# Kernel tuning notes

Measured on AMD Instinct MI355X. Metric: run time of the kernel, lower is better.

## Reference

```python
import jax, jax.numpy as jnp
import numpy as np

B, N, C, H = 2, 2048, 256, 8
HD = C // H  # 32


def _pairwise_sq_dist(x, y):
    # x,y: [B,N,3] -> [B,N,N] squared euclidean distance
    x2 = jnp.sum(x * x, axis=-1)  # [B,N]
    y2 = jnp.sum(y * y, axis=-1)  # [B,N]
    xy = jnp.einsum('bnd,bmd->bnm', x, y)
    return x2[:, :, None] + y2[:, None, :] - 2.0 * xy


def setup_inputs() -> dict:
    key = jax.random.key(0)
    ks = jax.random.split(key, 12)
    s = 0.02
    return {
        'feature': jax.random.normal(ks[0], (B, N, C), jnp.float32),
        'points': jax.random.normal(ks[1], (B, N, 3), jnp.float32),
        'Wq': jax.random.normal(ks[2], (C, H * HD), jnp.float32) * s,
        'bq': jnp.zeros((H * HD,), jnp.float32),
        'Wk': jax.random.normal(ks[3], (C, H * HD), jnp.float32) * s,
        'bk': jnp.zeros((H * HD,), jnp.float32),
        'Wv': jax.random.normal(ks[4], (C, H * HD), jnp.float32) * s,
        'bv': jnp.zeros((H * HD,), jnp.float32),
        'Wo': jax.random.normal(ks[5], (H * HD, C), jnp.float32) * s,
        'bo': jnp.zeros((C,), jnp.float32),
        'ln_g': jnp.ones((C,), jnp.float32),
        'ln_b': jnp.zeros((C,), jnp.float32),
    }


def reference(feature, points, Wq, bq, Wk, bk, Wv, bv, Wo, bo, ln_g, ln_b):
    xyz = points[..., 0:3]
    dist = _pairwise_sq_dist(xyz, xyz)  # [B,N,N] geometric bias

    q = (feature @ Wq + bq).reshape(B, N, H, HD)
    k = (feature @ Wk + bk).reshape(B, N, H, HD)
    v = (feature @ Wv + bv).reshape(B, N, H, HD)

    # distance-biased multi-head attention (Geoglobal_FPT)
    logits = jnp.einsum('bnhd,bmhd->bhnm', q, k) / jnp.sqrt(jnp.float32(HD))
    logits = logits - dist[:, None, :, :]  # closer points attend more
    attn = jax.nn.softmax(logits, axis=-1)
    out = jnp.einsum('bhnm,bmhd->bnhd', attn, v).reshape(B, N, H * HD)
    out = out @ Wo + bo

    # residual + post-LayerNorm
    f = feature + out
    mu = jnp.mean(f, axis=-1, keepdims=True)
    var = jnp.mean(jnp.square(f - mu), axis=-1, keepdims=True)
    f = (f - mu) * jax.lax.rsqrt(var + 1e-5) * ln_g + ln_b
    return f
```

## Files before the change

kernel.cpp:

```cpp
#include <hip/hip_runtime.h>
#include <hip/hip_bf16.h>

#define B_ 2
#define N_ 2048
#define C_ 256
#define H_ 8
#define HD_ 32

typedef __bf16 bhalf;
typedef bhalf bhalf8 __attribute__((ext_vector_type(8)));
typedef bhalf bhalf4 __attribute__((ext_vector_type(4)));
typedef float floatx4 __attribute__((ext_vector_type(4)));
typedef short short4v __attribute__((ext_vector_type(4)));

__device__ __forceinline__ floatx4 mfma16x16x16bf16(bhalf4 a, bhalf4 b, floatx4 c) {
#if __has_builtin(__builtin_amdgcn_mfma_f32_16x16x16_bf16)
    return __builtin_amdgcn_mfma_f32_16x16x16_bf16(a, b, c, 0, 0, 0);
#else
    return __builtin_amdgcn_mfma_f32_16x16x16bf16_1k(
        __builtin_bit_cast(short4v, a), __builtin_bit_cast(short4v, b), c, 0, 0, 0);
#endif
}

__global__ __launch_bounds__(256) void prep_all(
    const float* __restrict__ Wq, const float* __restrict__ Wk,
    const float* __restrict__ Wv, const float* __restrict__ Wo,
    const float* __restrict__ pts, const float* __restrict__ feat,
    bhalf* __restrict__ Wtb, bhalf* __restrict__ qext,
    bhalf* __restrict__ kext, bhalf* __restrict__ fb)
{
    __shared__ float T[64][65];
    const int bx = blockIdx.x;
    const int t = threadIdx.x;
    if (bx < 64) {
        const int wsel = bx >> 4;
        const float* W = wsel == 0 ? Wq : (wsel == 1 ? Wk : (wsel == 2 ? Wv : Wo));
        bhalf* dst = Wtb + (size_t)wsel * (C_ * C_);
        const int tile = bx & 15;
        const int kt = (tile >> 2) * 64, nt = (tile & 3) * 64;
        const int c4 = (t & 15) * 4;
#pragma unroll
        for (int i = 0; i < 4; ++i) {
            const int r = (t >> 4) + i * 16;
            const float4 w = *(const float4*)&W[(kt + r) * C_ + nt + c4];
            T[r][c4 + 0] = w.x; T[r][c4 + 1] = w.y; T[r][c4 + 2] = w.z; T[r][c4 + 3] = w.w;
        }
        __syncthreads();
#pragma unroll
        for (int i = 0; i < 4; ++i) {
            const int n = (t >> 4) + i * 16;
            bhalf4 o;
            o[0] = (bhalf)T[c4 + 0][n]; o[1] = (bhalf)T[c4 + 1][n];
            o[2] = (bhalf)T[c4 + 2][n]; o[3] = (bhalf)T[c4 + 3][n];
            *(bhalf4*)&dst[(nt + n) * C_ + kt + c4] = o;
        }
    } else if (bx < 80) {
        const int i = (bx - 64) * 256 + t;
        const float x = pts[i * 3 + 0], y = pts[i * 3 + 1], z = pts[i * 3 + 2];
        const float nn = x * x + y * y + z * z;
        const bhalf hi = (bhalf)nn;
        const bhalf lo = (bhalf)(nn - (float)hi);
        bhalf8 qe, ke;
        qe[0] = (bhalf)(2.f * x); qe[1] = (bhalf)(2.f * y); qe[2] = (bhalf)(2.f * z);
        qe[3] = (bhalf)(-(float)hi); qe[4] = (bhalf)(-(float)lo);
        qe[5] = (bhalf)1.f; qe[6] = (bhalf)1.f; qe[7] = (bhalf)0.f;
        ke[0] = (bhalf)x; ke[1] = (bhalf)y; ke[2] = (bhalf)z;
        ke[3] = (bhalf)1.f; ke[4] = (bhalf)1.f;
        ke[5] = (bhalf)(-(float)hi); ke[6] = (bhalf)(-(float)lo); ke[7] = (bhalf)0.f;
        *(bhalf8*)&qext[(size_t)i * 8] = qe;
        *(bhalf8*)&kext[(size_t)i * 8] = ke;
    } else {
        const int idx = ((bx - 80) * 256 + t) * 4;
        const float4 f = *(const float4*)&feat[idx];
        bhalf4 o;
        o[0] = (bhalf)f.x; o[1] = (bhalf)f.y; o[2] = (bhalf)f.z; o[3] = (bhalf)f.w;
        *(bhalf4*)&fb[idx] = o;
    }
}

__global__ __launch_bounds__(256) void qkv_gemm(
    const bhalf* __restrict__ fb, const bhalf* __restrict__ Wtb,
    const float* __restrict__ bq, const float* __restrict__ bk,
    const float* __restrict__ bv,
    bhalf* __restrict__ qs, bhalf* __restrict__ kg, bhalf* __restrict__ vt)
{
    __shared__ __align__(16) bhalf Alds[2][32][72];
    __shared__ __align__(16) bhalf Blds[2][64][72];

    const int tid = threadIdx.x;
    const int wave = tid >> 6, lane = tid & 63;
    const int quad = lane >> 4, l16 = lane & 15;
    const int m0 = blockIdx.x * 32;
    const int which = blockIdx.y >> 2;
    const int n0 = (blockIdx.y & 3) * 64;
    const bhalf* Wt = Wtb + (size_t)which * (C_ * C_);
    const int mw = (wave & 1) * 16;
    const int cw = (wave >> 1) * 32;

    const floatx4 zacc = {0.f, 0.f, 0.f, 0.f};
    floatx4 acc[2] = {zacc, zacc};

    const int arow = tid >> 3, aoff = (tid & 7) * 8;
    const int brow = tid >> 2, boff = (tid & 3) * 16;

    bhalf8 ra  = *(const bhalf8*)&fb[(m0 + arow) * C_ + aoff];
    bhalf8 rb0 = *(const bhalf8*)&Wt[(n0 + brow) * C_ + boff];
    bhalf8 rb1 = *(const bhalf8*)&Wt[(n0 + brow) * C_ + boff + 8];
    *(bhalf8*)&Alds[0][arow][aoff] = ra;
    *(bhalf8*)&Blds[0][brow][boff] = rb0;
    *(bhalf8*)&Blds[0][brow][boff + 8] = rb1;

    int cur = 0;
    for (int kci = 0; kci < 4; ++kci) {
        __syncthreads();
        if (kci < 3) {
            const int kc = (kci + 1) * 64;
            ra  = *(const bhalf8*)&fb[(m0 + arow) * C_ + kc + aoff];
            rb0 = *(const bhalf8*)&Wt[(n0 + brow) * C_ + kc + boff];
            rb1 = *(const bhalf8*)&Wt[(n0 + brow) * C_ + kc + boff + 8];
        }
        const bhalf8 a0 = *(const bhalf8*)&Alds[cur][mw + l16][quad * 8];
        const bhalf8 a1 = *(const bhalf8*)&Alds[cur][mw + l16][32 + quad * 8];
#pragma unroll
        for (int f = 0; f < 2; ++f) {
            const bhalf8 b0 = *(const bhalf8*)&Blds[cur][cw + f * 16 + l16][quad * 8];
            const bhalf8 b1 = *(const bhalf8*)&Blds[cur][cw + f * 16 + l16][32 + quad * 8];
            acc[f] = __builtin_amdgcn_mfma_f32_16x16x32_bf16(a0, b0, acc[f], 0, 0, 0);
            acc[f] = __builtin_amdgcn_mfma_f32_16x16x32_bf16(a1, b1, acc[f], 0, 0, 0);
        }
        if (kci < 3) {
            *(bhalf8*)&Alds[cur ^ 1][arow][aoff] = ra;
            *(bhalf8*)&Blds[cur ^ 1][brow][boff] = rb0;
            *(bhalf8*)&Blds[cur ^ 1][brow][boff + 8] = rb1;
        }
        cur ^= 1;
    }

    const float scale = 0.17677669529663687f;
    const float* bias = which == 0 ? bq : (which == 1 ? bk : bv);
#pragma unroll
    for (int f = 0; f < 2; ++f) {
        const int cg = n0 + cw + f * 16 + l16;
        const float bi = bias[cg];
        const int hh = cg >> 5, dd = cg & 31;
#pragma unroll
        for (int r = 0; r < 4; ++r) {
            const int m = m0 + mw + quad * 4 + r;
            const int bb = m >> 11, nn = m & (N_ - 1);
            const float val = acc[f][r] + bi;
            if (which == 0) {
                qs[((size_t)(bb * H_ + hh) * N_ + nn) * HD_ + dd] = (bhalf)(val * scale);
            } else if (which == 1) {
                kg[((size_t)(bb * H_ + hh) * N_ + nn) * HD_ + dd] = (bhalf)val;
            } else {
                vt[(((size_t)(bb * H_ + hh) * (N_ / 64) + (nn >> 6)) * HD_ + dd) * 64 + (nn & 63)] = (bhalf)val;
            }
        }
    }
}

__global__ __launch_bounds__(256) void attn_kernel(
    const bhalf* __restrict__ qs, const bhalf* __restrict__ kg,
    const bhalf* __restrict__ vt, const bhalf* __restrict__ qext,
    const bhalf* __restrict__ kext,
    bhalf* __restrict__ po, float* __restrict__ pl, int spbits)
{
    __shared__ __align__(16) bhalf Ks[2][64][40];
    __shared__ __align__(16) bhalf Vts[2][32][72];
    __shared__ __align__(16) bhalf Kes[2][64][8];

    const int tid = threadIdx.x;
    const int wave = tid >> 6, lane = tid & 63;
    const int quad = lane >> 4, l16 = lane & 15;
    const int n0 = blockIdx.x * 64;
    const int h = blockIdx.y;
    const int sp = blockIdx.z & ((1 << spbits) - 1);
    const int b = blockIdx.z >> spbits;
    const int bh = b * H_ + h;

    const int qrow = n0 + wave * 16 + l16;
    const bhalf8 bq_ = *(const bhalf8*)&qs[((size_t)bh * N_ + qrow) * HD_ + quad * 8];
    bhalf8 zv8;
#pragma unroll
    for (int j = 0; j < 8; ++j) zv8[j] = (bhalf)0.f;
    const bhalf8 bqe = (quad == 0)
        ? *(const bhalf8*)&qext[(size_t)(b * N_ + qrow) * 8] : zv8;

    const floatx4 zacc = {0.f, 0.f, 0.f, 0.f};
    floatx4 o0 = zacc, o1 = zacc;
    float ls = 0.f;

    const int skey = tid >> 2, sseg = tid & 3;
    const int vd = tid >> 3, vks = tid & 7;
    const int ekey = tid >> 1, eoff = (tid & 1) * 4;
    const int iters = (N_ >> spbits) / 64;
    const int mbase = sp * (N_ >> spbits);

    bhalf8 rk = *(const bhalf8*)&kg[((size_t)bh * N_ + mbase + skey) * HD_ + sseg * 8];
    bhalf8 rv = *(const bhalf8*)&vt[(((size_t)bh * (N_ / 64) + (mbase >> 6)) * HD_ + vd) * 64 + vks * 8];
    bhalf4 re;
    if (tid < 128) re = *(const bhalf4*)&kext[(size_t)(b * N_ + mbase + ekey) * 8 + eoff];
    *(bhalf8*)&Ks[0][skey][sseg * 8] = rk;
    *(bhalf8*)&Vts[0][vd][vks * 8] = rv;
    if (tid < 128) *(bhalf4*)&Kes[0][ekey][eoff] = re;

    int cur = 0;
    for (int it = 0; it < iters; ++it) {
        __syncthreads();
        if (it + 1 < iters) {
            const int m1 = mbase + (it + 1) * 64;
            rk = *(const bhalf8*)&kg[((size_t)bh * N_ + m1 + skey) * HD_ + sseg * 8];
            rv = *(const bhalf8*)&vt[(((size_t)bh * (N_ / 64) + (m1 >> 6)) * HD_ + vd) * 64 + vks * 8];
            if (tid < 128) re = *(const bhalf4*)&kext[(size_t)(b * N_ + m1 + ekey) * 8 + eoff];
        }
#pragma unroll
        for (int mt = 0; mt < 4; ++mt) {
            const bhalf8 ak_ = *(const bhalf8*)&Ks[cur][mt * 16 + l16][quad * 8];
            floatx4 st = __builtin_amdgcn_mfma_f32_16x16x32_bf16(ak_, bq_, zacc, 0, 0, 0);
            const bhalf8 ake = (quad == 0)
                ? *(const bhalf8*)&Kes[cur][mt * 16 + l16][0] : zv8;
            st = __builtin_amdgcn_mfma_f32_16x16x32_bf16(ake, bqe, st, 0, 0, 0);
            bhalf4 pt;
#pragma unroll
            for (int r = 0; r < 4; ++r) {
                const float p = __expf(st[r]);
                ls += p;
                pt[r] = (bhalf)p;
            }
            const bhalf4 av0 = *(const bhalf4*)&Vts[cur][l16][mt * 16 + quad * 4];
            const bhalf4 av1 = *(const bhalf4*)&Vts[cur][16 + l16][mt * 16 + quad * 4];
            o0 = mfma16x16x16bf16(av0, pt, o0);
            o1 = mfma16x16x16bf16(av1, pt, o1);
        }
        if (it + 1 < iters) {
            *(bhalf8*)&Ks[cur ^ 1][skey][sseg * 8] = rk;
            *(bhalf8*)&Vts[cur ^ 1][vd][vks * 8] = rv;
            if (tid < 128) *(bhalf4*)&Kes[cur ^ 1][ekey][eoff] = re;
        }
        cur ^= 1;
    }

    ls += __shfl_xor(ls, 16);
    ls += __shfl_xor(ls, 32);

    const size_t pobase = (size_t)sp * ((size_t)B_ * H_ * N_ * HD_) + (size_t)bh * N_ * HD_;
    bhalf4 w0, w1;
#pragma unroll
    for (int r = 0; r < 4; ++r) { w0[r] = (bhalf)o0[r]; w1[r] = (bhalf)o1[r]; }
    *(bhalf4*)&po[pobase + (size_t)qrow * HD_ + quad * 4] = w0;
    *(bhalf4*)&po[pobase + (size_t)qrow * HD_ + 16 + quad * 4] = w1;
    if (lane < 16)
        pl[(size_t)sp * (B_ * H_ * N_) + (size_t)bh * N_ + qrow] = ls;
}

__global__ __launch_bounds__(256) void outln_gemm(
    const bhalf* __restrict__ po, const float* __restrict__ pl,
    const bhalf* __restrict__ Wot, const float* __restrict__ bo,
    const float* __restrict__ feat, const float* __restrict__ g,
    const float* __restrict__ bb, float* __restrict__ out, int splits)
{
    __shared__ __align__(16) bhalf Alds[16][264];
    __shared__ __align__(16) bhalf Blds[2][256][40];
    __shared__ float rden[16][8];
    __shared__ float wsum[4][16][2];
    __shared__ float stats[16][2];

    const int tid = threadIdx.x;
    const int wave = tid >> 6, lane = tid & 63;
    const int quad = lane >> 4, l16 = lane & 15;
    const int row0 = blockIdx.x * 16;

    if (tid < 128) {
        const int m = tid >> 3, hh = tid & 7;
        const int grow = row0 + m;
        const int b = grow >> 11, n = grow & (N_ - 1);
        float den = 0.f;
        for (int sp = 0; sp < splits; ++sp)
            den += pl[(size_t)sp * (B_ * H_ * N_) + (size_t)(b * H_ + hh) * N_ + n];
        rden[m][hh] = 1.f / den;
    }
    __syncthreads();

    {
        const int m = tid >> 4, seg = tid & 15;
        const int hh = seg >> 1, d0 = (seg & 1) * 16;
        const int grow = row0 + m;
        const int b = grow >> 11, n = grow & (N_ - 1);
        const size_t idx = ((size_t)(b * H_ + hh) * N_ + n) * HD_ + d0;
        float num[16];
#pragma unroll
        for (int j = 0; j < 16; ++j) num[j] = 0.f;
        for (int sp = 0; sp < splits; ++sp) {
            const bhalf8 p0 = *(const bhalf8*)&po[(size_t)sp * ((size_t)B_ * H_ * N_ * HD_) + idx];
            const bhalf8 p1 = *(const bhalf8*)&po[(size_t)sp * ((size_t)B_ * H_ * N_ * HD_) + idx + 8];
#pragma unroll
            for (int j = 0; j < 8; ++j) { num[j] += (float)p0[j]; num[8 + j] += (float)p1[j]; }
        }
        const float r = rden[m][hh];
        bhalf8 a0, a1;
#pragma unroll
        for (int j = 0; j < 8; ++j) { a0[j] = (bhalf)(num[j] * r); a1[j] = (bhalf)(num[8 + j] * r); }
        *(bhalf8*)&Alds[m][seg * 16] = a0;
        *(bhalf8*)&Alds[m][seg * 16 + 8] = a1;
    }

    const floatx4 zacc = {0.f, 0.f, 0.f, 0.f};
    floatx4 acc[4];
#pragma unroll
    for (int f = 0; f < 4; ++f) acc[f] = zacc;

    bhalf8 rb0 = *(const bhalf8*)&Wot[tid * C_ + 0];
    bhalf8 rb1 = *(const bhalf8*)&Wot[tid * C_ + 8];
    bhalf8 rb2 = *(const bhalf8*)&Wot[tid * C_ + 16];
    bhalf8 rb3 = *(const bhalf8*)&Wot[tid * C_ + 24];
    *(bhalf8*)&Blds[0][tid][0]  = rb0;
    *(bhalf8*)&Blds[0][tid][8]  = rb1;
    *(bhalf8*)&Blds[0][tid][16] = rb2;
    *(bhalf8*)&Blds[0][tid][24] = rb3;

    int cur = 0;
    for (int kci = 0; kci < 8; ++kci) {
        __syncthreads();
        if (kci < 7) {
            const bhalf* wp = &Wot[tid * C_ + (kci + 1) * 32];
            rb0 = *(const bhalf8*)(wp);
            rb1 = *(const bhalf8*)(wp + 8);
            rb2 = *(const bhalf8*)(wp + 16);
            rb3 = *(const bhalf8*)(wp + 24);
        }
        const bhalf8 af = *(const bhalf8*)&Alds[l16][kci * 32 + quad * 8];
#pragma unroll
        for (int f = 0; f < 4; ++f) {
            const bhalf8 bfr = *(const bhalf8*)&Blds[cur][wave * 64 + f * 16 + l16][quad * 8];
            acc[f] = __builtin_amdgcn_mfma_f32_16x16x32_bf16(af, bfr, acc[f], 0, 0, 0);
        }
        if (kci < 7) {
            *(bhalf8*)&Blds[cur ^ 1][tid][0]  = rb0;
            *(bhalf8*)&Blds[cur ^ 1][tid][8]  = rb1;
            *(bhalf8*)&Blds[cur ^ 1][tid][16] = rb2;
            *(bhalf8*)&Blds[cur ^ 1][tid][24] = rb3;
        }
        cur ^= 1;
    }

    float fv[4][4];
    float s1[4] = {0.f, 0.f, 0.f, 0.f}, s2[4] = {0.f, 0.f, 0.f, 0.f};
#pragma unroll
    for (int f = 0; f < 4; ++f) {
        const int col = wave * 64 + f * 16 + l16;
        const float bic = bo[col];
#pragma unroll
        for (int r = 0; r < 4; ++r) {
            const int m = quad * 4 + r;
            const float x = acc[f][r] + bic + feat[(row0 + m) * C_ + col];
            fv[f][r] = x;
            s1[r] += x; s2[r] += x * x;
        }
    }
#pragma unroll
    for (int r = 0; r < 4; ++r) {
        for (int o = 1; o < 16; o <<= 1) {
            s1[r] += __shfl_xor(s1[r], o);
            s2[r] += __shfl_xor(s2[r], o);
        }
    }
    if (l16 == 0) {
#pragma unroll
        for (int r = 0; r < 4; ++r) {
            wsum[wave][quad * 4 + r][0] = s1[r];
            wsum[wave][quad * 4 + r][1] = s2[r];
        }
    }
    __syncthreads();
    if (tid < 16) {
        float a = 0.f, bsq = 0.f;
#pragma unroll
        for (int w = 0; w < 4; ++w) { a += wsum[w][tid][0]; bsq += wsum[w][tid][1]; }
        const float mu = a * (1.f / C_);
        const float var = bsq * (1.f / C_) - mu * mu;
        stats[tid][0] = mu;
        stats[tid][1] = rsqrtf(var + 1e-5f);
    }
    __syncthreads();
#pragma unroll
    for (int f = 0; f < 4; ++f) {
        const int col = wave * 64 + f * 16 + l16;
        const float gc = g[col], bc = bb[col];
#pragma unroll
        for (int r = 0; r < 4; ++r) {
            const int m = quad * 4 + r;
            out[(row0 + m) * C_ + col] = (fv[f][r] - stats[m][0]) * stats[m][1] * gc + bc;
        }
    }
}

extern "C" void kernel_launch(void* const* d_in, const int* in_sizes, int n_in,
                              void* d_out, int out_size, void* d_ws, size_t ws_size,
                              hipStream_t stream) {
    const float* feat = (const float*)d_in[0];
    const float* pts  = (const float*)d_in[1];
    const float* Wq   = (const float*)d_in[2];
    const float* bq   = (const float*)d_in[3];
    const float* Wk   = (const float*)d_in[4];
    const float* bk   = (const float*)d_in[5];
    const float* Wv   = (const float*)d_in[6];
    const float* bv   = (const float*)d_in[7];
    const float* Wo   = (const float*)d_in[8];
    const float* bo   = (const float*)d_in[9];
    const float* lng  = (const float*)d_in[10];
    const float* lnb  = (const float*)d_in[11];

    char* w = (char*)d_ws;
    bhalf* Wtb  = (bhalf*)(w);
    bhalf* fb   = (bhalf*)(w + 524288);
    bhalf* qs   = (bhalf*)(w + 2621440);
    bhalf* kg   = (bhalf*)(w + 4718592);
    bhalf* vtp  = (bhalf*)(w + 6815744);
    bhalf* qext = (bhalf*)(w + 8912896);
    bhalf* kext = (bhalf*)(w + 8978432);
    float* pl   = (float*)(w + 9043968);
    bhalf* po   = (bhalf*)(w + 9568256);

    const int spbits = (ws_size >= 17956864u) ? 2 : 1;
    const int splits = 1 << spbits;

    prep_all<<<80 + B_ * N_ * C_ / 1024, 256, 0, stream>>>(
        Wq, Wk, Wv, Wo, pts, feat, Wtb, qext, kext, fb);
    qkv_gemm<<<dim3(B_ * N_ / 32, 12), 256, 0, stream>>>(
        fb, Wtb, bq, bk, bv, qs, kg, vtp);
    attn_kernel<<<dim3(N_ / 64, H_, B_ << spbits), 256, 0, stream>>>(
        qs, kg, vtp, qext, kext, po, pl, spbits);
    outln_gemm<<<B_ * N_ / 16, 256, 0, stream>>>(
        po, pl, Wtb + 3 * (C_ * C_), bo, feat, lng, lnb, (float*)d_out, splits);
}
```

Baseline: 125.9 us.

## Process two query tiles per wave in attention and vectorize V stores

Each attention block now covers 128 query rows instead of 64. Each wave computes two 16-row query tiles against the same K/V tiles in shared memory, so every K and V LDS read and global load is reused twice and the grid is halved. Separately, the QKV GEMM epilogue writes the transposed V output as one 4-element vector store instead of four scalar stores. The cost is more accumulator registers per thread and fewer blocks in flight, which could lower occupancy.

```diff
diff --git a/kernel.cpp b/kernel.cpp
--- a/kernel.cpp
+++ b/kernel.cpp
@@ -143,17 +143,21 @@
         const int cg = n0 + cw + f * 16 + l16;
         const float bi = bias[cg];
         const int hh = cg >> 5, dd = cg & 31;
-#pragma unroll
-        for (int r = 0; r < 4; ++r) {
-            const int m = m0 + mw + quad * 4 + r;
-            const int bb = m >> 11, nn = m & (N_ - 1);
-            const float val = acc[f][r] + bi;
-            if (which == 0) {
-                qs[((size_t)(bb * H_ + hh) * N_ + nn) * HD_ + dd] = (bhalf)(val * scale);
-            } else if (which == 1) {
-                kg[((size_t)(bb * H_ + hh) * N_ + nn) * HD_ + dd] = (bhalf)val;
-            } else {
-                vt[(((size_t)(bb * H_ + hh) * (N_ / 64) + (nn >> 6)) * HD_ + dd) * 64 + (nn & 63)] = (bhalf)val;
+        const int m = m0 + mw + quad * 4;
+        const int bb = m >> 11, nn = m & (N_ - 1);
+        if (which == 2) {
+            bhalf4 vw;
+#pragma unroll
+            for (int r = 0; r < 4; ++r) vw[r] = (bhalf)(acc[f][r] + bi);
+            *(bhalf4*)&vt[(((size_t)(bb * H_ + hh) * (N_ / 64) + (nn >> 6)) * HD_ + dd) * 64 + (nn & 63)] = vw;
+        } else {
+#pragma unroll
+            for (int r = 0; r < 4; ++r) {
+                const float val = acc[f][r] + bi;
+                if (which == 0)
+                    qs[((size_t)(bb * H_ + hh) * N_ + nn + r) * HD_ + dd] = (bhalf)(val * scale);
+                else
+                    kg[((size_t)(bb * H_ + hh) * N_ + nn + r) * HD_ + dd] = (bhalf)val;
             }
         }
     }
@@ -172,23 +176,27 @@
     const int tid = threadIdx.x;
     const int wave = tid >> 6, lane = tid & 63;
     const int quad = lane >> 4, l16 = lane & 15;
-    const int n0 = blockIdx.x * 64;
+    const int n0 = blockIdx.x * 128;
     const int h = blockIdx.y;
     const int sp = blockIdx.z & ((1 << spbits) - 1);
     const int b = blockIdx.z >> spbits;
     const int bh = b * H_ + h;
 
-    const int qrow = n0 + wave * 16 + l16;
-    const bhalf8 bq_ = *(const bhalf8*)&qs[((size_t)bh * N_ + qrow) * HD_ + quad * 8];
+    const int qrow0 = n0 + wave * 32 + l16;
+    const int qrow1 = qrow0 + 16;
+    const bhalf8 bq0 = *(const bhalf8*)&qs[((size_t)bh * N_ + qrow0) * HD_ + quad * 8];
+    const bhalf8 bq1 = *(const bhalf8*)&qs[((size_t)bh * N_ + qrow1) * HD_ + quad * 8];
     bhalf8 zv8;
 #pragma unroll
     for (int j = 0; j < 8; ++j) zv8[j] = (bhalf)0.f;
-    const bhalf8 bqe = (quad == 0)
-        ? *(const bhalf8*)&qext[(size_t)(b * N_ + qrow) * 8] : zv8;
+    const bhalf8 bqe0 = (quad == 0)
+        ? *(const bhalf8*)&qext[(size_t)(b * N_ + qrow0) * 8] : zv8;
+    const bhalf8 bqe1 = (quad == 0)
+        ? *(const bhalf8*)&qext[(size_t)(b * N_ + qrow1) * 8] : zv8;
 
     const floatx4 zacc = {0.f, 0.f, 0.f, 0.f};
-    floatx4 o0 = zacc, o1 = zacc;
-    float ls = 0.f;
+    floatx4 o00 = zacc, o01 = zacc, o10 = zacc, o11 = zacc;
+    float ls0 = 0.f, ls1 = 0.f;
 
     const int skey = tid >> 2, sseg = tid & 3;
     const int vd = tid >> 3, vks = tid & 7;
@@ -216,21 +224,26 @@
 #pragma unroll
         for (int mt = 0; mt < 4; ++mt) {
             const bhalf8 ak_ = *(const bhalf8*)&Ks[cur][mt * 16 + l16][quad * 8];
-            floatx4 st = __builtin_amdgcn_mfma_f32_16x16x32_bf16(ak_, bq_, zacc, 0, 0, 0);
             const bhalf8 ake = (quad == 0)
                 ? *(const bhalf8*)&Kes[cur][mt * 16 + l16][0] : zv8;
-            st = __builtin_amdgcn_mfma_f32_16x16x32_bf16(ake, bqe, st, 0, 0, 0);
-            bhalf4 pt;
+            floatx4 st0 = __builtin_amdgcn_mfma_f32_16x16x32_bf16(ak_, bq0, zacc, 0, 0, 0);
+            st0 = __builtin_amdgcn_mfma_f32_16x16x32_bf16(ake, bqe0, st0, 0, 0, 0);
+            floatx4 st1 = __builtin_amdgcn_mfma_f32_16x16x32_bf16(ak_, bq1, zacc, 0, 0, 0);
+            st1 = __builtin_amdgcn_mfma_f32_16x16x32_bf16(ake, bqe1, st1, 0, 0, 0);
+            bhalf4 pt0, pt1;
 #pragma unroll
             for (int r = 0; r < 4; ++r) {
-                const float p = __expf(st[r]);
-                ls += p;
-                pt[r] = (bhalf)p;
+                const float p0 = __expf(st0[r]);
+                const float p1 = __expf(st1[r]);
+                ls0 += p0; ls1 += p1;
+                pt0[r] = (bhalf)p0; pt1[r] = (bhalf)p1;
             }
             const bhalf4 av0 = *(const bhalf4*)&Vts[cur][l16][mt * 16 + quad * 4];
             const bhalf4 av1 = *(const bhalf4*)&Vts[cur][16 + l16][mt * 16 + quad * 4];
-            o0 = mfma16x16x16bf16(av0, pt, o0);
-            o1 = mfma16x16x16bf16(av1, pt, o1);
+            o00 = mfma16x16x16bf16(av0, pt0, o00);
+            o01 = mfma16x16x16bf16(av1, pt0, o01);
+            o10 = mfma16x16x16bf16(av0, pt1, o10);
+            o11 = mfma16x16x16bf16(av1, pt1, o11);
         }
         if (it + 1 < iters) {
             *(bhalf8*)&Ks[cur ^ 1][skey][sseg * 8] = rk;
@@ -240,17 +253,24 @@
         cur ^= 1;
     }
 
-    ls += __shfl_xor(ls, 16);
-    ls += __shfl_xor(ls, 32);
+    ls0 += __shfl_xor(ls0, 16); ls0 += __shfl_xor(ls0, 32);
+    ls1 += __shfl_xor(ls1, 16); ls1 += __shfl_xor(ls1, 32);
 
     const size_t pobase = (size_t)sp * ((size_t)B_ * H_ * N_ * HD_) + (size_t)bh * N_ * HD_;
-    bhalf4 w0, w1;
-#pragma unroll
-    for (int r = 0; r < 4; ++r) { w0[r] = (bhalf)o0[r]; w1[r] = (bhalf)o1[r]; }
-    *(bhalf4*)&po[pobase + (size_t)qrow * HD_ + quad * 4] = w0;
-    *(bhalf4*)&po[pobase + (size_t)qrow * HD_ + 16 + quad * 4] = w1;
+    bhalf4 w00, w01, w10, w11;
+#pragma unroll
+    for (int r = 0; r < 4; ++r) {
+        w00[r] = (bhalf)o00[r]; w01[r] = (bhalf)o01[r];
+        w10[r] = (bhalf)o10[r]; w11[r] = (bhalf)o11[r];
+    }
+    *(bhalf4*)&po[pobase + (size_t)qrow0 * HD_ + quad * 4] = w00;
+    *(bhalf4*)&po[pobase + (size_t)qrow0 * HD_ + 16 + quad * 4] = w01;
+    *(bhalf4*)&po[pobase + (size_t)qrow1 * HD_ + quad * 4] = w10;
+    *(bhalf4*)&po[pobase + (size_t)qrow1 * HD_ + 16 + quad * 4] = w11;
     if (lane < 16)
-        pl[(size_t)sp * (B_ * H_ * N_) + (size_t)bh * N_ + qrow] = ls;
+        pl[(size_t)sp * (B_ * H_ * N_) + (size_t)bh * N_ + qrow0] = ls0;
+    else if (lane < 32)
+        pl[(size_t)sp * (B_ * H_ * N_) + (size_t)bh * N_ + qrow1] = ls1;
 }
 
 __global__ __launch_bounds__(256) void outln_gemm(
@@ -428,7 +448,7 @@
         Wq, Wk, Wv, Wo, pts, feat, Wtb, qext, kext, fb);
     qkv_gemm<<<dim3(B_ * N_ / 32, 12), 256, 0, stream>>>(
         fb, Wtb, bq, bk, bv, qs, kg, vtp);
-    attn_kernel<<<dim3(N_ / 64, H_, B_ << spbits), 256, 0, stream>>>(
+    attn_kernel<<<dim3(N_ / 128, H_, B_ << spbits), 256, 0, stream>>>(
         qs, kg, vtp, qext, kext, po, pl, spbits);
     outln_gemm<<<B_ * N_ / 16, 256, 0, stream>>>(
         po, pl, Wtb + 3 * (C_ * C_), bo, feat, lng, lnb, (float*)d_out, splits);
```

After: 122.1 us. -3.0%, faster.

## Widen attention query tile per block, raise key split count, halve out-LN row tile

Applied to the files above, without the earlier changes.

The attention kernel now has each wave handle 64 query rows (4 groups of 16) instead of 16, so each K/V tile staged in shared memory is reused across 4x more queries. The grid shrinks in x, and the key dimension is split up to 8 ways when workspace allows, to keep parallelism. The output GEMM+LayerNorm kernel uses 8-row blocks with zero padding to spread work over more blocks, and the V store in the QKV GEMM is vectorised to 4-wide. In exchange, register pressure rises from the 8 accumulators per wave, and po/pl traffic plus the reduction grow with more splits.

```diff
diff --git a/kernel.cpp b/kernel.cpp
--- a/kernel.cpp
+++ b/kernel.cpp
@@ -143,17 +143,21 @@
         const int cg = n0 + cw + f * 16 + l16;
         const float bi = bias[cg];
         const int hh = cg >> 5, dd = cg & 31;
-#pragma unroll
-        for (int r = 0; r < 4; ++r) {
-            const int m = m0 + mw + quad * 4 + r;
-            const int bb = m >> 11, nn = m & (N_ - 1);
-            const float val = acc[f][r] + bi;
-            if (which == 0) {
-                qs[((size_t)(bb * H_ + hh) * N_ + nn) * HD_ + dd] = (bhalf)(val * scale);
-            } else if (which == 1) {
-                kg[((size_t)(bb * H_ + hh) * N_ + nn) * HD_ + dd] = (bhalf)val;
-            } else {
-                vt[(((size_t)(bb * H_ + hh) * (N_ / 64) + (nn >> 6)) * HD_ + dd) * 64 + (nn & 63)] = (bhalf)val;
+        const int m = m0 + mw + quad * 4;
+        const int bb = m >> 11, nn = m & (N_ - 1);
+        if (which == 2) {
+            bhalf4 vw;
+#pragma unroll
+            for (int r = 0; r < 4; ++r) vw[r] = (bhalf)(acc[f][r] + bi);
+            *(bhalf4*)&vt[(((size_t)(bb * H_ + hh) * (N_ / 64) + (nn >> 6)) * HD_ + dd) * 64 + (nn & 63)] = vw;
+        } else {
+#pragma unroll
+            for (int r = 0; r < 4; ++r) {
+                const float val = acc[f][r] + bi;
+                if (which == 0)
+                    qs[((size_t)(bb * H_ + hh) * N_ + nn + r) * HD_ + dd] = (bhalf)(val * scale);
+                else
+                    kg[((size_t)(bb * H_ + hh) * N_ + nn + r) * HD_ + dd] = (bhalf)val;
             }
         }
     }
@@ -172,23 +176,30 @@
     const int tid = threadIdx.x;
     const int wave = tid >> 6, lane = tid & 63;
     const int quad = lane >> 4, l16 = lane & 15;
-    const int n0 = blockIdx.x * 64;
+    const int n0 = blockIdx.x * 256;
     const int h = blockIdx.y;
     const int sp = blockIdx.z & ((1 << spbits) - 1);
     const int b = blockIdx.z >> spbits;
     const int bh = b * H_ + h;
 
-    const int qrow = n0 + wave * 16 + l16;
-    const bhalf8 bq_ = *(const bhalf8*)&qs[((size_t)bh * N_ + qrow) * HD_ + quad * 8];
     bhalf8 zv8;
 #pragma unroll
     for (int j = 0; j < 8; ++j) zv8[j] = (bhalf)0.f;
-    const bhalf8 bqe = (quad == 0)
-        ? *(const bhalf8*)&qext[(size_t)(b * N_ + qrow) * 8] : zv8;
+
+    bhalf8 bq[4], bqe[4];
+#pragma unroll
+    for (int g = 0; g < 4; ++g) {
+        const int qrow = n0 + wave * 64 + g * 16 + l16;
+        bq[g] = *(const bhalf8*)&qs[((size_t)bh * N_ + qrow) * HD_ + quad * 8];
+        bqe[g] = (quad == 0)
+            ? *(const bhalf8*)&qext[(size_t)(b * N_ + qrow) * 8] : zv8;
+    }
 
     const floatx4 zacc = {0.f, 0.f, 0.f, 0.f};
-    floatx4 o0 = zacc, o1 = zacc;
-    float ls = 0.f;
+    floatx4 o[4][2];
+#pragma unroll
+    for (int g = 0; g < 4; ++g) { o[g][0] = zacc; o[g][1] = zacc; }
+    float ls[4] = {0.f, 0.f, 0.f, 0.f};
 
     const int skey = tid >> 2, sseg = tid & 3;
     const int vd = tid >> 3, vks = tid & 7;
@@ -216,21 +227,24 @@
 #pragma unroll
         for (int mt = 0; mt < 4; ++mt) {
             const bhalf8 ak_ = *(const bhalf8*)&Ks[cur][mt * 16 + l16][quad * 8];
-            floatx4 st = __builtin_amdgcn_mfma_f32_16x16x32_bf16(ak_, bq_, zacc, 0, 0, 0);
             const bhalf8 ake = (quad == 0)
                 ? *(const bhalf8*)&Kes[cur][mt * 16 + l16][0] : zv8;
-            st = __builtin_amdgcn_mfma_f32_16x16x32_bf16(ake, bqe, st, 0, 0, 0);
-            bhalf4 pt;
-#pragma unroll
-            for (int r = 0; r < 4; ++r) {
-                const float p = __expf(st[r]);
-                ls += p;
-                pt[r] = (bhalf)p;
-            }
             const bhalf4 av0 = *(const bhalf4*)&Vts[cur][l16][mt * 16 + quad * 4];
             const bhalf4 av1 = *(const bhalf4*)&Vts[cur][16 + l16][mt * 16 + quad * 4];
-            o0 = mfma16x16x16bf16(av0, pt, o0);
-            o1 = mfma16x16x16bf16(av1, pt, o1);
+#pragma unroll
+            for (int g = 0; g < 4; ++g) {
+                floatx4 st = __builtin_amdgcn_mfma_f32_16x16x32_bf16(ak_, bq[g], zacc, 0, 0, 0);
+                st = __builtin_amdgcn_mfma_f32_16x16x32_bf16(ake, bqe[g], st, 0, 0, 0);
+                bhalf4 pt;
+#pragma unroll
+                for (int r = 0; r < 4; ++r) {
+                    const float p = __expf(st[r]);
+                    ls[g] += p;
+                    pt[r] = (bhalf)p;
+                }
+                o[g][0] = mfma16x16x16bf16(av0, pt, o[g][0]);
+                o[g][1] = mfma16x16x16bf16(av1, pt, o[g][1]);
+            }
         }
         if (it + 1 < iters) {
             *(bhalf8*)&Ks[cur ^ 1][skey][sseg * 8] = rk;
@@ -240,17 +254,21 @@
         cur ^= 1;
     }
 
-    ls += __shfl_xor(ls, 16);
-    ls += __shfl_xor(ls, 32);
-
     const size_t pobase = (size_t)sp * ((size_t)B_ * H_ * N_ * HD_) + (size_t)bh * N_ * HD_;
-    bhalf4 w0, w1;
-#pragma unroll
-    for (int r = 0; r < 4; ++r) { w0[r] = (bhalf)o0[r]; w1[r] = (bhalf)o1[r]; }
-    *(bhalf4*)&po[pobase + (size_t)qrow * HD_ + quad * 4] = w0;
-    *(bhalf4*)&po[pobase + (size_t)qrow * HD_ + 16 + quad * 4] = w1;
-    if (lane < 16)
-        pl[(size_t)sp * (B_ * H_ * N_) + (size_t)bh * N_ + qrow] = ls;
+    const size_t plbase = (size_t)sp * (B_ * H_ * N_) + (size_t)bh * N_;
+#pragma unroll
+    for (int g = 0; g < 4; ++g) {
+        ls[g] += __shfl_xor(ls[g], 16);
+        ls[g] += __shfl_xor(ls[g], 32);
+        const int qrow = n0 + wave * 64 + g * 16 + l16;
+        bhalf4 w0, w1;
+#pragma unroll
+        for (int r = 0; r < 4; ++r) { w0[r] = (bhalf)o[g][0][r]; w1[r] = (bhalf)o[g][1][r]; }
+        *(bhalf4*)&po[pobase + (size_t)qrow * HD_ + quad * 4] = w0;
+        *(bhalf4*)&po[pobase + (size_t)qrow * HD_ + 16 + quad * 4] = w1;
+        if (lane < 16)
+            pl[plbase + qrow] = ls[g];
+    }
 }
 
 __global__ __launch_bounds__(256) void outln_gemm(
@@ -261,16 +279,16 @@
 {
     __shared__ __align__(16) bhalf Alds[16][264];
     __shared__ __align__(16) bhalf Blds[2][256][40];
-    __shared__ float rden[16][8];
-    __shared__ float wsum[4][16][2];
-    __shared__ float stats[16][2];
+    __shared__ float rden[8][8];
+    __shared__ float wsum[4][8][2];
+    __shared__ float stats[8][2];
 
     const int tid = threadIdx.x;
     const int wave = tid >> 6, lane = tid & 63;
     const int quad = lane >> 4, l16 = lane & 15;
-    const int row0 = blockIdx.x * 16;
-
-    if (tid < 128) {
+    const int row0 = blockIdx.x * 8;
+
+    if (tid < 64) {
         const int m = tid >> 3, hh = tid & 7;
         const int grow = row0 + m;
         const int b = grow >> 11, n = grow & (N_ - 1);
@@ -283,25 +301,33 @@
 
     {
         const int m = tid >> 4, seg = tid & 15;
-        const int hh = seg >> 1, d0 = (seg & 1) * 16;
-        const int grow = row0 + m;
-        const int b = grow >> 11, n = grow & (N_ - 1);
-        const size_t idx = ((size_t)(b * H_ + hh) * N_ + n) * HD_ + d0;
-        float num[16];
-#pragma unroll
-        for (int j = 0; j < 16; ++j) num[j] = 0.f;
-        for (int sp = 0; sp < splits; ++sp) {
-            const bhalf8 p0 = *(const bhalf8*)&po[(size_t)sp * ((size_t)B_ * H_ * N_ * HD_) + idx];
-            const bhalf8 p1 = *(const bhalf8*)&po[(size_t)sp * ((size_t)B_ * H_ * N_ * HD_) + idx + 8];
-#pragma unroll
-            for (int j = 0; j < 8; ++j) { num[j] += (float)p0[j]; num[8 + j] += (float)p1[j]; }
-        }
-        const float r = rden[m][hh];
-        bhalf8 a0, a1;
-#pragma unroll
-        for (int j = 0; j < 8; ++j) { a0[j] = (bhalf)(num[j] * r); a1[j] = (bhalf)(num[8 + j] * r); }
-        *(bhalf8*)&Alds[m][seg * 16] = a0;
-        *(bhalf8*)&Alds[m][seg * 16 + 8] = a1;
+        bhalf8 z;
+#pragma unroll
+        for (int j = 0; j < 8; ++j) z[j] = (bhalf)0.f;
+        if (m < 8) {
+            const int hh = seg >> 1, d0 = (seg & 1) * 16;
+            const int grow = row0 + m;
+            const int b = grow >> 11, n = grow & (N_ - 1);
+            const size_t idx = ((size_t)(b * H_ + hh) * N_ + n) * HD_ + d0;
+            float num[16];
+#pragma unroll
+            for (int j = 0; j < 16; ++j) num[j] = 0.f;
+            for (int sp = 0; sp < splits; ++sp) {
+                const bhalf8 p0 = *(const bhalf8*)&po[(size_t)sp * ((size_t)B_ * H_ * N_ * HD_) + idx];
+                const bhalf8 p1 = *(const bhalf8*)&po[(size_t)sp * ((size_t)B_ * H_ * N_ * HD_) + idx + 8];
+#pragma unroll
+                for (int j = 0; j < 8; ++j) { num[j] += (float)p0[j]; num[8 + j] += (float)p1[j]; }
+            }
+            const float r = rden[m][hh];
+            bhalf8 a0, a1;
+#pragma unroll
+            for (int j = 0; j < 8; ++j) { a0[j] = (bhalf)(num[j] * r); a1[j] = (bhalf)(num[8 + j] * r); }
+            *(bhalf8*)&Alds[m][seg * 16] = a0;
+            *(bhalf8*)&Alds[m][seg * 16 + 8] = a1;
+        } else {
+            *(bhalf8*)&Alds[m][seg * 16] = z;
+            *(bhalf8*)&Alds[m][seg * 16 + 8] = z;
+        }
     }
 
     const floatx4 zacc = {0.f, 0.f, 0.f, 0.f};
@@ -352,7 +378,8 @@
 #pragma unroll
         for (int r = 0; r < 4; ++r) {
             const int m = quad * 4 + r;
-            const float x = acc[f][r] + bic + feat[(row0 + m) * C_ + col];
+            float x = 0.f;
+            if (m < 8) x = acc[f][r] + bic + feat[(row0 + m) * C_ + col];
             fv[f][r] = x;
             s1[r] += x; s2[r] += x * x;
         }
@@ -364,7 +391,7 @@
             s2[r] += __shfl_xor(s2[r], o);
         }
     }
-    if (l16 == 0) {
+    if (l16 == 0 && quad < 2) {
 #pragma unroll
         for (int r = 0; r < 4; ++r) {
             wsum[wave][quad * 4 + r][0] = s1[r];
@@ -372,7 +399,7 @@
         }
     }
     __syncthreads();
-    if (tid < 16) {
+    if (tid < 8) {
         float a = 0.f, bsq = 0.f;
 #pragma unroll
         for (int w = 0; w < 4; ++w) { a += wsum[w][tid][0]; bsq += wsum[w][tid][1]; }
@@ -382,14 +409,16 @@
         stats[tid][1] = rsqrtf(var + 1e-5f);
     }
     __syncthreads();
-#pragma unroll
-    for (int f = 0; f < 4; ++f) {
-        const int col = wave * 64 + f * 16 + l16;
-        const float gc = g[col], bc = bb[col];
-#pragma unroll
-        for (int r = 0; r < 4; ++r) {
-            const int m = quad * 4 + r;
-            out[(row0 + m) * C_ + col] = (fv[f][r] - stats[m][0]) * stats[m][1] * gc + bc;
+    if (quad < 2) {
+#pragma unroll
+        for (int f = 0; f < 4; ++f) {
+            const int col = wave * 64 + f * 16 + l16;
+            const float gc = g[col], bc = bb[col];
+#pragma unroll
+            for (int r = 0; r < 4; ++r) {
+                const int m = quad * 4 + r;
+                out[(row0 + m) * C_ + col] = (fv[f][r] - stats[m][0]) * stats[m][1] * gc + bc;
+            }
         }
     }
 }
@@ -419,17 +448,17 @@
     bhalf* qext = (bhalf*)(w + 8912896);
     bhalf* kext = (bhalf*)(w + 8978432);
     float* pl   = (float*)(w + 9043968);
-    bhalf* po   = (bhalf*)(w + 9568256);
-
-    const int spbits = (ws_size >= 17956864u) ? 2 : 1;
+    bhalf* po   = (bhalf*)(w + 10092544);
+
+    const int spbits = (ws_size >= 26869760u) ? 3 : ((ws_size >= 18481152u) ? 2 : 1);
     const int splits = 1 << spbits;
 
     prep_all<<<80 + B_ * N_ * C_ / 1024, 256, 0, stream>>>(
         Wq, Wk, Wv, Wo, pts, feat, Wtb, qext, kext, fb);
     qkv_gemm<<<dim3(B_ * N_ / 32, 12), 256, 0, stream>>>(
         fb, Wtb, bq, bk, bv, qs, kg, vtp);
-    attn_kernel<<<dim3(N_ / 64, H_, B_ << spbits), 256, 0, stream>>>(
+    attn_kernel<<<dim3(N_ / 256, H_, B_ << spbits), 256, 0, stream>>>(
         qs, kg, vtp, qext, kext, po, pl, spbits);
-    outln_gemm<<<B_ * N_ / 16, 256, 0, stream>>>(
+    outln_gemm<<<B_ * N_ / 8, 256, 0, stream>>>(
         po, pl, Wtb + 3 * (C_ * C_), bo, feat, lng, lnb, (float*)d_out, splits);
 }
```

Measured after the change: 131.2 us. 4.3% more time.
